# Performance work log

Hardware: AMD Instinct MI355X
Metric: run time of the kernel (lower is better)

## Reference

```python
import jax, jax.numpy as jnp
import numpy as np

B, S, T = 32, 2048, 768
NH, DH, DHID = 8, 96, 384  # num_heads, head_dim, hidden_dim=4*head_dim


def setup_inputs() -> dict:
    key = jax.random.key(0)
    k = jax.random.split(key, 7)
    token_embeddings = jax.random.normal(k[0], (B, S, T), dtype=jnp.float32)
    attention_mask = jnp.ones((B, S), dtype=jnp.float32)
    # per-head Linear params, stacked on a leading head axis (PyTorch default-ish init scale)
    P_w = jax.random.normal(k[1], (NH, T, DH), dtype=jnp.float32) * (1.0 / np.sqrt(T))
    P_b = jax.random.normal(k[2], (NH, DH), dtype=jnp.float32) * 0.01
    W1_w = jax.random.normal(k[3], (NH, DH, DHID), dtype=jnp.float32) * (1.0 / np.sqrt(DH))
    W1_b = jax.random.normal(k[4], (NH, DHID), dtype=jnp.float32) * 0.01
    W2_w = jax.random.normal(k[5], (NH, DHID, DH), dtype=jnp.float32) * (1.0 / np.sqrt(DHID))
    W2_b = jax.random.normal(k[6], (NH, DH), dtype=jnp.float32) * 0.01
    return {
        'token_embeddings': token_embeddings,
        'attention_mask': attention_mask,
        'P_w': P_w, 'P_b': P_b,
        'W1_w': W1_w, 'W1_b': W1_b,
        'W2_w': W2_w, 'W2_b': W2_b,
    }


def reference(token_embeddings, attention_mask, P_w, P_b, W1_w, W1_b, W2_w, W2_b):
    # Batched over heads instead of the original Python loop; same math per head.
    # H_i = P_i(H): (B, NH, S, DH)
    Hi = jnp.einsum('bst,htd->bhsd', token_embeddings, P_w) + P_b[None, :, None, :]
    # A_i = W2_i(relu(W1_i(H_i))): (B, NH, S, DH)
    A = jax.nn.relu(jnp.einsum('bhsd,hde->bhse', Hi, W1_w) + W1_b[None, :, None, :])
    A = jnp.einsum('bhse,hed->bhsd', A, W2_w) + W2_b[None, :, None, :]
    # masked softmax over the sequence axis (log(mask) adds -inf at padded tokens)
    log_mask = jnp.log(attention_mask)[:, None, :, None]  # (B,1,S,1)
    A = jax.nn.softmax(A + log_mask, axis=2)
    # weighted sum over tokens: (B, NH, DH)
    v = jnp.sum(Hi * A, axis=2)
    # concat heads -> (B, NH*DH) == (B, sentence_dim)
    return v.reshape(v.shape[0], NH * DH)
```

## Files before the change

### kernel.cpp

```cpp
#include <hip/hip_runtime.h>
#include <cstdint>
#include <cstddef>

#define Bsz   32
#define Ssz   2048
#define Tsz   768
#define NH    8
#define DH    96
#define DHID  384
#define Ncols (NH*DH)

using u16 = unsigned short;
typedef __bf16 bf16x8 __attribute__((ext_vector_type(8)));
typedef __bf16 bf16x4 __attribute__((ext_vector_type(4)));
typedef float  f32x4  __attribute__((ext_vector_type(4)));

__device__ __forceinline__ u16 f2bn(float f) {
  __bf16 h = (__bf16)f;
  return __builtin_bit_cast(u16, h);
}
__device__ __forceinline__ float b2f(u16 u) {
  return __builtin_bit_cast(float, (uint32_t)u << 16);
}

typedef const __attribute__((address_space(1))) void* gas_t;
typedef __attribute__((address_space(3))) void* las_t;
__device__ __forceinline__ void gload16(const void* g, void* s) {
  __builtin_amdgcn_global_load_lds((gas_t)g, (las_t)s, 16, 0, 0);
}

__global__ __launch_bounds__(256) void k_pack(const float* __restrict__ Pw,
    const float* __restrict__ W1w, const float* __restrict__ W2w,
    u16* __restrict__ B1t, u16* __restrict__ W1t, u16* __restrict__ W2t)
{
  int i = blockIdx.x * 256 + threadIdx.x;
  if (i < 589824) {
    int n = i / 768, k = i % 768;
    int h = n / 96, d = n % 96;
    B1t[i] = f2bn(Pw[(size_t)h*73728 + (size_t)k*96 + d]);
  } else if (i < 589824 + 294912) {
    int j = i - 589824;
    int h = j / 36864, r = j % 36864;
    int n = r / 96, k = r % 96;
    W1t[j] = f2bn(W1w[(size_t)h*36864 + (size_t)k*384 + n]);
  } else if (i < 589824 + 2*294912) {
    int q = i - 589824 - 294912;
    int h = q / 36864, r = q % 36864;
    int n = r / 384, k = r % 384;
    W2t[q] = f2bn(W2w[(size_t)h*36864 + (size_t)k*96 + n]);
  }
}

__global__ __launch_bounds__(256) void k_gemm1(const float* __restrict__ emb,
    const u16* __restrict__ B1t, const float* __restrict__ Pb, u16* __restrict__ Hi)
{
  __shared__ float As[128*64];
  __shared__ u16   Bs[128*64];
  const int tid  = threadIdx.x;
  const int lane = tid & 63;
  const int w    = tid >> 6;
  const int wr = w >> 1, wc = w & 1;
  const int L = blockIdx.x;
  const int widx = (L & 7) * 384 + (L >> 3);
  const int bm = widx / 6, bn = widx % 6;
  const int l15 = lane & 15, lg = lane >> 4;

  const int arow_in = lane >> 4;
  const int achunk  = lane & 15;
  const int brow_in = lane >> 3;
  const int bchunk  = lane & 7;

  f32x4 acc[4][4] = {};

  for (int kt = 0; kt < 12; ++kt) {
    const int k0 = kt * 64;
    #pragma unroll
    for (int i = 0; i < 8; ++i) {
      const int row = (w*8 + i)*4 + arow_in;
      const int lc  = achunk ^ (row & 15);
      gload16(emb + (size_t)(bm*128 + row)*Tsz + k0 + lc*4,
              &As[(w*8 + i)*256]);
    }
    #pragma unroll
    for (int i = 0; i < 4; ++i) {
      const int row = (w*4 + i)*8 + brow_in;
      const int lc  = bchunk ^ brow_in;
      gload16(B1t + (size_t)(bn*128 + row)*Tsz + k0 + lc*8,
              &Bs[(w*4 + i)*512]);
    }
    __syncthreads();

    bf16x8 b[4][2];
    #pragma unroll
    for (int c = 0; c < 4; ++c) {
      const int Rb = wc*64 + c*16 + l15;
      #pragma unroll
      for (int kk = 0; kk < 2; ++kk)
        b[c][kk] = *reinterpret_cast<const bf16x8*>(
            &Bs[Rb*64 + (((kk*4 + lg) ^ (l15 & 7))*8)]);
    }
    #pragma unroll
    for (int r = 0; r < 4; ++r) {
      const int R = wr*64 + r*16 + l15;
      #pragma unroll
      for (int kk = 0; kk < 2; ++kk) {
        const int c0 = kk*8 + lg*2;
        f32x4 fa0 = *reinterpret_cast<const f32x4*>(&As[R*64 + ((c0    ) ^ l15)*4]);
        f32x4 fa1 = *reinterpret_cast<const f32x4*>(&As[R*64 + ((c0 + 1) ^ l15)*4]);
        bf16x8 af;
        af[0] = (__bf16)fa0[0]; af[1] = (__bf16)fa0[1];
        af[2] = (__bf16)fa0[2]; af[3] = (__bf16)fa0[3];
        af[4] = (__bf16)fa1[0]; af[5] = (__bf16)fa1[1];
        af[6] = (__bf16)fa1[2]; af[7] = (__bf16)fa1[3];
        #pragma unroll
        for (int c = 0; c < 4; ++c)
          acc[r][c] = __builtin_amdgcn_mfma_f32_16x16x32_bf16(af, b[c][kk], acc[r][c], 0, 0, 0);
      }
    }
    __syncthreads();
  }
  #pragma unroll
  for (int c = 0; c < 4; ++c) {
    int col = bn*128 + wc*64 + c*16 + l15;
    float bias = Pb[col];
    #pragma unroll
    for (int r = 0; r < 4; ++r) {
      int row0 = bm*128 + wr*64 + r*16 + lg*4;
      #pragma unroll
      for (int j = 0; j < 4; ++j)
        Hi[(size_t)(row0 + j)*Ncols + col] = f2bn(acc[r][c][j] + bias);
    }
  }
}

__global__ __launch_bounds__(256, 1) void k_ffn_pool(
    const u16* __restrict__ Hi, const u16* __restrict__ W1t, const u16* __restrict__ W2t,
    const float* __restrict__ b1, const float* __restrict__ b2v, const float* __restrict__ mask,
    float* __restrict__ out)
{
  __shared__ u16 W2s[96][392];
  __shared__ u16 Zb[4][2][16][40];
  __shared__ float mb[4][96], lb[4][96], ab[4][96];

  const int tid = threadIdx.x, lane = tid & 63, w = tid >> 6;
  const int l15 = lane & 15, lg = lane >> 4;
  const int h = blockIdx.x, b = blockIdx.y;

  const u16* W1h = W1t + (size_t)h * DHID * DH;
  const u16* W2h = W2t + (size_t)h * DH * DHID;
  const float* b1h = b1 + h * DHID;

  for (int i = tid; i < 96*48; i += 256) {
    int r = i / 48, g = i % 48;
    uint4 v = *reinterpret_cast<const uint4*>(W2h + (size_t)r*DHID + g*8);
    *reinterpret_cast<uint4*>(&W2s[r][g*8]) = v;
  }
  __syncthreads();

  float b2s[6];
  #pragma unroll
  for (int ct = 0; ct < 6; ++ct) b2s[ct] = b2v[h*DH + ct*16 + l15];

  float Mr[6], Lr[6], Ar[6];
  #pragma unroll
  for (int ct = 0; ct < 6; ++ct) { Mr[ct] = -3.4e38f; Lr[ct] = 0.f; Ar[ct] = 0.f; }

  #pragma unroll 1
  for (int pass = 0; pass < 8; ++pass) {
    const size_t prow = (size_t)b*Ssz + (size_t)w*512 + (size_t)pass*64;

    bf16x8 hifr[4][3];
    #pragma unroll
    for (int s = 0; s < 4; ++s)
      #pragma unroll
      for (int ks = 0; ks < 3; ++ks)
        hifr[s][ks] = *reinterpret_cast<const bf16x8*>(
            Hi + (prow + s*16 + l15)*Ncols + h*DH + ks*32 + lg*8);

    f32x4 lgt[4][6] = {};

    #pragma unroll 2
    for (int c = 0; c < 12; ++c) {
      bf16x8 a1c[2][3];
      #pragma unroll
      for (int t = 0; t < 2; ++t)
        #pragma unroll
        for (int ks = 0; ks < 3; ++ks)
          a1c[t][ks] = *reinterpret_cast<const bf16x8*>(
              W1h + (size_t)(c*32 + t*16 + l15)*DH + ks*32 + lg*8);
      float4 bc0 = *reinterpret_cast<const float4*>(b1h + c*32 + lg*4);
      float4 bc1 = *reinterpret_cast<const float4*>(b1h + c*32 + 16 + lg*4);
      bf16x8 b2fr[6];
      #pragma unroll
      for (int ct = 0; ct < 6; ++ct)
        b2fr[ct] = *reinterpret_cast<const bf16x8*>(&W2s[ct*16 + l15][c*32 + lg*8]);

      #pragma unroll
      for (int bi = 0; bi < 2; ++bi) {
        f32x4 z[2][2];
        #pragma unroll
        for (int sl = 0; sl < 2; ++sl) {
          z[sl][0] = f32x4{}; z[sl][1] = f32x4{};
          #pragma unroll
          for (int ks = 0; ks < 3; ++ks) {
            z[sl][0] = __builtin_amdgcn_mfma_f32_16x16x32_bf16(a1c[0][ks], hifr[bi*2+sl][ks], z[sl][0], 0, 0, 0);
            z[sl][1] = __builtin_amdgcn_mfma_f32_16x16x32_bf16(a1c[1][ks], hifr[bi*2+sl][ks], z[sl][1], 0, 0, 0);
          }
        }
        #pragma unroll
        for (int sl = 0; sl < 2; ++sl) {
          bf16x4 p0, p1;
          p0[0] = (__bf16)fmaxf(z[sl][0][0] + bc0.x, 0.f);
          p0[1] = (__bf16)fmaxf(z[sl][0][1] + bc0.y, 0.f);
          p0[2] = (__bf16)fmaxf(z[sl][0][2] + bc0.z, 0.f);
          p0[3] = (__bf16)fmaxf(z[sl][0][3] + bc0.w, 0.f);
          p1[0] = (__bf16)fmaxf(z[sl][1][0] + bc1.x, 0.f);
          p1[1] = (__bf16)fmaxf(z[sl][1][1] + bc1.y, 0.f);
          p1[2] = (__bf16)fmaxf(z[sl][1][2] + bc1.z, 0.f);
          p1[3] = (__bf16)fmaxf(z[sl][1][3] + bc1.w, 0.f);
          *reinterpret_cast<uint2*>(&Zb[w][sl][l15][lg*4])      = __builtin_bit_cast(uint2, p0);
          *reinterpret_cast<uint2*>(&Zb[w][sl][l15][16 + lg*4]) = __builtin_bit_cast(uint2, p1);
        }
        #pragma unroll
        for (int sl = 0; sl < 2; ++sl) {
          bf16x8 zf = *reinterpret_cast<const bf16x8*>(&Zb[w][sl][l15][lg*8]);
          #pragma unroll
          for (int ct = 0; ct < 6; ++ct)
            lgt[bi*2+sl][ct] = __builtin_amdgcn_mfma_f32_16x16x32_bf16(zf, b2fr[ct], lgt[bi*2+sl][ct], 0, 0, 0);
        }
      }
    }

    float lmv[4][4];
    #pragma unroll
    for (int s = 0; s < 4; ++s) {
      float4 mk = *reinterpret_cast<const float4*>(&mask[prow + s*16 + lg*4]);
      lmv[s][0] = __logf(mk.x); lmv[s][1] = __logf(mk.y);
      lmv[s][2] = __logf(mk.z); lmv[s][3] = __logf(mk.w);
    }
    float G[4][6][4];
    #pragma unroll
    for (int s = 0; s < 4; ++s)
      #pragma unroll
      for (int ct = 0; ct < 6; ++ct)
        #pragma unroll
        for (int j = 0; j < 4; ++j)
          G[s][ct][j] = b2f(Hi[(prow + s*16 + lg*4 + j)*Ncols + h*DH + ct*16 + l15]);

    #pragma unroll
    for (int ct = 0; ct < 6; ++ct) {
      float av[4][4];
      float m16 = -3.4e38f;
      #pragma unroll
      for (int s = 0; s < 4; ++s)
        #pragma unroll
        for (int j = 0; j < 4; ++j) {
          av[s][j] = lgt[s][ct][j] + b2s[ct] + lmv[s][j];
          m16 = fmaxf(m16, av[s][j]);
        }
      m16 = fmaxf(m16, __shfl_xor(m16, 16));
      m16 = fmaxf(m16, __shfl_xor(m16, 32));
      float l16 = 0.f, a16 = 0.f;
      #pragma unroll
      for (int s = 0; s < 4; ++s)
        #pragma unroll
        for (int j = 0; j < 4; ++j) {
          float p = __expf(av[s][j] - m16);
          l16 += p;
          a16 += p * G[s][ct][j];
        }
      l16 += __shfl_xor(l16, 16); l16 += __shfl_xor(l16, 32);
      a16 += __shfl_xor(a16, 16); a16 += __shfl_xor(a16, 32);
      float M2 = fmaxf(Mr[ct], m16);
      float eo = __expf(Mr[ct] - M2), en = __expf(m16 - M2);
      Lr[ct] = Lr[ct]*eo + l16*en;
      Ar[ct] = Ar[ct]*eo + a16*en;
      Mr[ct] = M2;
    }
  }

  if (lane < 16) {
    #pragma unroll
    for (int ct = 0; ct < 6; ++ct) {
      mb[w][ct*16 + l15] = Mr[ct];
      lb[w][ct*16 + l15] = Lr[ct];
      ab[w][ct*16 + l15] = Ar[ct];
    }
  }
  __syncthreads();
  if (tid < 96) {
    float m = fmaxf(fmaxf(mb[0][tid], mb[1][tid]), fmaxf(mb[2][tid], mb[3][tid]));
    float l = 0.f, a = 0.f;
    #pragma unroll
    for (int q = 0; q < 4; ++q) {
      float sc = __expf(mb[q][tid] - m);
      l += lb[q][tid] * sc;
      a += ab[q][tid] * sc;
    }
    out[(size_t)b * Ncols + h*DH + tid] = a / l;
  }
}

extern "C" void kernel_launch(void* const* d_in, const int* in_sizes, int n_in,
                              void* d_out, int out_size, void* d_ws, size_t ws_size,
                              hipStream_t stream)
{
  const float* emb  = (const float*)d_in[0];
  const float* mask = (const float*)d_in[1];
  const float* Pw   = (const float*)d_in[2];
  const float* Pb   = (const float*)d_in[3];
  const float* W1w  = (const float*)d_in[4];
  const float* W1b  = (const float*)d_in[5];
  const float* W2w  = (const float*)d_in[6];
  const float* W2b  = (const float*)d_in[7];
  float* out = (float*)d_out;

  char* ws = (char*)d_ws;
  u16*   Hi  = (u16*)(ws);
  u16*   B1t = (u16*)(ws + 100663296ull);
  u16*   W1t = (u16*)(ws + 101842944ull);
  u16*   W2t = (u16*)(ws + 102432768ull);

  k_pack<<<dim3(4608), dim3(256), 0, stream>>>(Pw, W1w, W2w, B1t, W1t, W2t);
  k_gemm1<<<dim3(3072), dim3(256), 0, stream>>>(emb, B1t, Pb, Hi);
  k_ffn_pool<<<dim3(8, 32), dim3(256), 0, stream>>>(Hi, W1t, W2t, W1b, W2b, mask, out);
}
```

Before: 284.1 us.

## Enlarge gemm1 M tile to 256 and convert activations to bf16 once at LDS fill

The projection GEMM now computes 256x128 tiles per block instead of 128x128, which halves the grid and the number of times each B tile is loaded. The fp32 embedding rows are loaded into registers, converted to bf16 once and stored into LDS with an XOR swizzle, so the MFMA loop no longer repeats the fp32-to-bf16 conversion for every output column tile. The trade-off is twice as many accumulators and the loss of the asynchronous direct-to-LDS load for A. The launch bounds request two blocks per CU, which may squeeze registers.

```diff
diff --git a/kernel.cpp b/kernel.cpp
--- a/kernel.cpp
+++ b/kernel.cpp
@@ -51,36 +51,29 @@
   }
 }
 
-__global__ __launch_bounds__(256) void k_gemm1(const float* __restrict__ emb,
+__global__ __launch_bounds__(256, 2) void k_gemm1(const float* __restrict__ emb,
     const u16* __restrict__ B1t, const float* __restrict__ Pb, u16* __restrict__ Hi)
 {
-  __shared__ float As[128*64];
-  __shared__ u16   Bs[128*64];
+  __shared__ u16 As[256*64];
+  __shared__ u16 Bs[128*64];
   const int tid  = threadIdx.x;
   const int lane = tid & 63;
   const int w    = tid >> 6;
   const int wr = w >> 1, wc = w & 1;
   const int L = blockIdx.x;
-  const int widx = (L & 7) * 384 + (L >> 3);
+  const int widx = (L & 7) * 192 + (L >> 3);
   const int bm = widx / 6, bn = widx % 6;
   const int l15 = lane & 15, lg = lane >> 4;
 
-  const int arow_in = lane >> 4;
-  const int achunk  = lane & 15;
+  const int srow   = lane >> 3;
+  const int schunk = lane & 7;
   const int brow_in = lane >> 3;
   const int bchunk  = lane & 7;
 
-  f32x4 acc[4][4] = {};
+  f32x4 acc[8][4] = {};
 
   for (int kt = 0; kt < 12; ++kt) {
     const int k0 = kt * 64;
-    #pragma unroll
-    for (int i = 0; i < 8; ++i) {
-      const int row = (w*8 + i)*4 + arow_in;
-      const int lc  = achunk ^ (row & 15);
-      gload16(emb + (size_t)(bm*128 + row)*Tsz + k0 + lc*4,
-              &As[(w*8 + i)*256]);
-    }
     #pragma unroll
     for (int i = 0; i < 4; ++i) {
       const int row = (w*4 + i)*8 + brow_in;
@@ -88,34 +81,40 @@
       gload16(B1t + (size_t)(bn*128 + row)*Tsz + k0 + lc*8,
               &Bs[(w*4 + i)*512]);
     }
+    #pragma unroll
+    for (int i = 0; i < 8; ++i) {
+      const int row = w*64 + i*8 + srow;
+      const float* src = emb + (size_t)(bm*256 + row)*Tsz + k0 + schunk*8;
+      float4 v0 = *reinterpret_cast<const float4*>(src);
+      float4 v1 = *reinterpret_cast<const float4*>(src + 4);
+      bf16x8 af;
+      af[0] = (__bf16)v0.x; af[1] = (__bf16)v0.y; af[2] = (__bf16)v0.z; af[3] = (__bf16)v0.w;
+      af[4] = (__bf16)v1.x; af[5] = (__bf16)v1.y; af[6] = (__bf16)v1.z; af[7] = (__bf16)v1.w;
+      const int phys = schunk ^ (row & 7);
+      *reinterpret_cast<bf16x8*>(&As[row*64 + phys*8]) = af;
+    }
     __syncthreads();
 
-    bf16x8 b[4][2];
-    #pragma unroll
-    for (int c = 0; c < 4; ++c) {
-      const int Rb = wc*64 + c*16 + l15;
-      #pragma unroll
-      for (int kk = 0; kk < 2; ++kk)
-        b[c][kk] = *reinterpret_cast<const bf16x8*>(
-            &Bs[Rb*64 + (((kk*4 + lg) ^ (l15 & 7))*8)]);
-    }
-    #pragma unroll
-    for (int r = 0; r < 4; ++r) {
-      const int R = wr*64 + r*16 + l15;
-      #pragma unroll
-      for (int kk = 0; kk < 2; ++kk) {
-        const int c0 = kk*8 + lg*2;
-        f32x4 fa0 = *reinterpret_cast<const f32x4*>(&As[R*64 + ((c0    ) ^ l15)*4]);
-        f32x4 fa1 = *reinterpret_cast<const f32x4*>(&As[R*64 + ((c0 + 1) ^ l15)*4]);
-        bf16x8 af;
-        af[0] = (__bf16)fa0[0]; af[1] = (__bf16)fa0[1];
-        af[2] = (__bf16)fa0[2]; af[3] = (__bf16)fa0[3];
-        af[4] = (__bf16)fa1[0]; af[5] = (__bf16)fa1[1];
-        af[6] = (__bf16)fa1[2]; af[7] = (__bf16)fa1[3];
+    #pragma unroll
+    for (int kk = 0; kk < 2; ++kk) {
+      const int clog = kk*4 + lg;
+      bf16x8 b[4];
+      #pragma unroll
+      for (int c = 0; c < 4; ++c) {
+        const int Rb = wc*64 + c*16 + l15;
+        b[c] = *reinterpret_cast<const bf16x8*>(&Bs[Rb*64 + (clog ^ (Rb & 7))*8]);
+      }
+      bf16x8 a[8];
+      #pragma unroll
+      for (int m = 0; m < 8; ++m) {
+        const int R = wr*128 + m*16 + l15;
+        a[m] = *reinterpret_cast<const bf16x8*>(&As[R*64 + (clog ^ (R & 7))*8]);
+      }
+      #pragma unroll
+      for (int m = 0; m < 8; ++m)
         #pragma unroll
         for (int c = 0; c < 4; ++c)
-          acc[r][c] = __builtin_amdgcn_mfma_f32_16x16x32_bf16(af, b[c][kk], acc[r][c], 0, 0, 0);
-      }
+          acc[m][c] = __builtin_amdgcn_mfma_f32_16x16x32_bf16(a[m], b[c], acc[m][c], 0, 0, 0);
     }
     __syncthreads();
   }
@@ -124,11 +123,11 @@
     int col = bn*128 + wc*64 + c*16 + l15;
     float bias = Pb[col];
     #pragma unroll
-    for (int r = 0; r < 4; ++r) {
-      int row0 = bm*128 + wr*64 + r*16 + lg*4;
+    for (int m = 0; m < 8; ++m) {
+      int row0 = bm*256 + wr*128 + m*16 + lg*4;
       #pragma unroll
       for (int j = 0; j < 4; ++j)
-        Hi[(size_t)(row0 + j)*Ncols + col] = f2bn(acc[r][c][j] + bias);
+        Hi[(size_t)(row0 + j)*Ncols + col] = f2bn(acc[m][c][j] + bias);
     }
   }
 }
@@ -322,6 +321,6 @@
   u16*   W2t = (u16*)(ws + 102432768ull);
 
   k_pack<<<dim3(4608), dim3(256), 0, stream>>>(Pw, W1w, W2w, B1t, W1t, W2t);
-  k_gemm1<<<dim3(3072), dim3(256), 0, stream>>>(emb, B1t, Pb, Hi);
+  k_gemm1<<<dim3(1536), dim3(256), 0, stream>>>(emb, B1t, Pb, Hi);
   k_ffn_pool<<<dim3(8, 32), dim3(256), 0, stream>>>(Hi, W1t, W2t, W1b, W2b, mask, out);
 }
```

Result: no change. 284.0 us (-0.0%).
